# Optimization experiments

Hardware: AMD Instinct MI355X
Metric: run time of the kernel (lower is better)

## Reference

```python
import jax, jax.numpy as jnp
import numpy as np

NUM_HEADS = 16
DEPTH = 0


def rotate_half(x):
    x1, x2 = jnp.split(x, 2, axis=-1)
    return jnp.concatenate((-x2, x1), axis=-1)


def rotary_tables(seq_len, rot_dim, dtype):
    # RotaryEmbedding(dim=rot_dim): inv_freq over even indices of rot_dim
    inv_freq = 1.0 / (10000.0 ** (jnp.arange(0, rot_dim, 2, dtype=jnp.float32) / rot_dim))
    freqs = jnp.arange(seq_len, dtype=jnp.float32)[:, None] * inv_freq[None, :]  # [N, rot_dim/2]
    emb = jnp.concatenate((freqs, freqs), axis=-1)  # [N, rot_dim]
    return emb.astype(dtype), jnp.cos(emb).astype(dtype), jnp.sin(emb).astype(dtype)


def setup_inputs() -> dict:
    key = jax.random.key(0)
    ks = jax.random.split(key, 7)
    B, N, C = 1, 2048, 1024
    hd = C // NUM_HEADS
    std_qkv = (1.0 / C) ** 0.5
    std_proj = (1.0 / (2 * C)) ** 0.5
    return {
        "x": jax.random.normal(ks[0], (B, N, C), dtype=jnp.float32),
        "W_qkv": jax.random.normal(ks[1], (6 * C, C), dtype=jnp.float32) * std_qkv,
        "W_proj": jax.random.normal(ks[2], (C, 2 * C), dtype=jnp.float32) * std_proj,
        "lambda_q1": jax.random.normal(ks[3], (hd,), dtype=jnp.float32) * 0.1,
        "lambda_q2": jax.random.normal(ks[4], (hd,), dtype=jnp.float32) * 0.1,
        "lambda_k1": jax.random.normal(ks[5], (hd,), dtype=jnp.float32) * 0.1,
        "lambda_k2": jax.random.normal(ks[6], (hd,), dtype=jnp.float32) * 0.1,
    }


def reference(x, W_qkv, W_proj, lambda_q1, lambda_q2, lambda_k1, lambda_k2):
    B, N, C = x.shape
    H = NUM_HEADS
    hd = C // H
    scale = hd ** -0.5
    lambda_init = 0.8 - 0.6 * np.exp(-0.3 * DEPTH)

    qkv = jnp.einsum('bnc,dc->bnd', x, W_qkv)               # [B,N,6C]
    qkv = qkv.reshape(B, N, 6, H, hd).transpose(2, 0, 3, 1, 4)  # [6,B,H,N,hd]
    q = jnp.concatenate((qkv[0], qkv[1]), axis=-1)          # [B,H,N,2hd]
    k = jnp.concatenate((qkv[2], qkv[3]), axis=-1)
    v = jnp.concatenate((qkv[4], qkv[5]), axis=-1)

    _, cos, sin = rotary_tables(N, 2 * hd, x.dtype)          # [N,2hd]
    q = q * cos + rotate_half(q) * sin
    k = k * cos + rotate_half(k) * sin

    q1, q2 = jnp.split(q, 2, axis=-1)                        # [B,H,N,hd] each
    k1, k2 = jnp.split(k, 2, axis=-1)

    attn1 = jnp.einsum('bhid,bhjd->bhij', q1, k1) * scale
    attn2 = jnp.einsum('bhid,bhjd->bhij', q2, k2) * scale

    lam1 = jnp.exp(jnp.sum(lambda_q1 * lambda_k1))
    lam2 = jnp.exp(jnp.sum(lambda_q2 * lambda_k2))
    lam = (lam1 - lam2 + lambda_init).astype(x.dtype)

    probs = jax.nn.softmax(attn1, axis=-1) - lam * jax.nn.softmax(attn2, axis=-1)
    out = jnp.einsum('bhij,bhjd->bhid', probs, v)            # [B,H,N,2hd]
    out = out.transpose(0, 2, 1, 3).reshape(B, N, 2 * C)
    out = jnp.einsum('bnd,cd->bnc', out, W_proj)             # [B,N,C]
    return out
```

## Files before the change

kernel.cpp:

```cpp
#include <hip/hip_runtime.h>

using bf16_t = __bf16;
typedef __bf16 bf16x4 __attribute__((ext_vector_type(4)));
typedef __bf16 bf16x8 __attribute__((ext_vector_type(8)));
typedef float floatx4 __attribute__((ext_vector_type(4)));

#define MFMA_BF16(a, b, c) __builtin_amdgcn_mfma_f32_16x16x32_bf16((a), (b), (c), 0, 0, 0)

__device__ __forceinline__ void async_ld16(bf16_t* lds_dst, const bf16_t* g_src) {
    __builtin_amdgcn_global_load_lds(
        (const __attribute__((address_space(1))) void*)g_src,
        (__attribute__((address_space(3))) void*)lds_dst, 16, 0, 0);
}

__global__ __launch_bounds__(256) void cast_all(const float* __restrict__ x,
                                                const float* __restrict__ Wqkv,
                                                const float* __restrict__ Wproj,
                                                const float* __restrict__ lq1,
                                                const float* __restrict__ lq2,
                                                const float* __restrict__ lk1,
                                                const float* __restrict__ lk2,
                                                bf16_t* __restrict__ xb,
                                                bf16_t* __restrict__ Wqkvb,
                                                bf16_t* __restrict__ Wprojb,
                                                float* __restrict__ lamp) {
    const int b = blockIdx.x;
    if (b == 5120) {
        int l = threadIdx.x;
        if (l < 64) {
            float p1 = lq1[l] * lk1[l];
            float p2 = lq2[l] * lk2[l];
            #pragma unroll
            for (int d = 1; d < 64; d <<= 1) {
                p1 += __shfl_xor(p1, d);
                p2 += __shfl_xor(p2, d);
            }
            if (l == 0) *lamp = expf(p1) - expf(p2) + 0.2f;
        }
        return;
    }
    const float* src;
    bf16_t* dst;
    size_t i;
    if (b < 1024)      { src = x;     dst = xb;     i = (size_t)b * 256 + threadIdx.x; }
    else if (b < 4096) { src = Wqkv;  dst = Wqkvb;  i = (size_t)(b - 1024) * 256 + threadIdx.x; }
    else               { src = Wproj; dst = Wprojb; i = (size_t)(b - 4096) * 256 + threadIdx.x; }
    const floatx4 a = *(const floatx4*)(src + i * 8);
    const floatx4 c = *(const floatx4*)(src + i * 8 + 4);
    bf16x8 r;
    r[0] = (bf16_t)a[0]; r[1] = (bf16_t)a[1]; r[2] = (bf16_t)a[2]; r[3] = (bf16_t)a[3];
    r[4] = (bf16_t)c[0]; r[5] = (bf16_t)c[1]; r[6] = (bf16_t)c[2]; r[7] = (bf16_t)c[3];
    *(bf16x8*)(dst + i * 8) = r;
}

__global__ __launch_bounds__(256) void gemm_qkv_rot(const bf16_t* __restrict__ A,
                                                    const bf16_t* __restrict__ B,
                                                    bf16_t* __restrict__ Qb,
                                                    bf16_t* __restrict__ Kb,
                                                    bf16_t* __restrict__ Vt) {
    constexpr int K = 1024, BM = 128, BK = 32;
    __shared__ __align__(16) bf16_t As[2][BM * BK];
    __shared__ __align__(16) bf16_t Bs[2][BM * BK];
    const int t = threadIdx.x;
    const int lane = t & 63, wave = t >> 6;
    const int q4 = lane >> 4, m16 = lane & 15;
    const int mblk = blockIdx.y * BM;
    const int p = blockIdx.x >> 4, hh = blockIdx.x & 15;
    const int pbase = p * 2048 + hh * 64;
    const int wr = wave >> 1, wc = wave & 1;

    auto stage = [&](int buf, int k0) {
        #pragma unroll
        for (int rr = 0; rr < 2; ++rr) {
            int f = rr * 256 + t;
            async_ld16(&As[buf][f * 8], &A[(size_t)(mblk + (f >> 2)) * K + k0 + (f & 3) * 8]);
        }
        #pragma unroll
        for (int rr = 0; rr < 2; ++rr) {
            int f = rr * 256 + t;
            int rp = f >> 2, jt = rp >> 4;
            int Brow = pbase + (jt & 1) * 1024 + ((jt >> 1) * 16) + (rp & 15);
            async_ld16(&Bs[buf][f * 8], &B[(size_t)Brow * K + k0 + (f & 3) * 8]);
        }
    };

    floatx4 acc[4][4] = {};
    stage(0, 0);

    for (int it = 0; it < 32; ++it) {
        const int cur = it & 1;
        __syncthreads();
        if (it + 1 < 32) stage(cur ^ 1, (it + 1) * 32);

        bf16x8 a[4], b[4];
        #pragma unroll
        for (int i = 0; i < 4; ++i)
            a[i] = *(const bf16x8*)&As[cur][(wr * 64 + i * 16 + m16) * 32 + q4 * 8];
        #pragma unroll
        for (int j = 0; j < 4; ++j)
            b[j] = *(const bf16x8*)&Bs[cur][(wc * 64 + j * 16 + m16) * 32 + q4 * 8];
        __builtin_amdgcn_s_setprio(1);
        #pragma unroll
        for (int i = 0; i < 4; ++i)
            #pragma unroll
            for (int j = 0; j < 4; ++j)
                acc[i][j] = MFMA_BF16(a[i], b[j], acc[i][j]);
        __builtin_amdgcn_s_setprio(0);
    }

    if (p < 2) {
        bf16_t* dst = (p == 0) ? Qb : Kb;
        #pragma unroll
        for (int i = 0; i < 4; ++i) {
            int mbase = mblk + wr * 64 + i * 16 + q4 * 4;
            #pragma unroll
            for (int jp = 0; jp < 2; ++jp) {
                int e = (wc * 2 + jp) * 16 + m16;
                float invf = exp2f(-(float)e * (13.287712379549449f / 64.0f));
                #pragma unroll
                for (int r = 0; r < 4; ++r) {
                    int m = mbase + r;
                    float sn, cs;
                    sincosf((float)m * invf, &sn, &cs);
                    float v1 = acc[i][2 * jp][r], v2 = acc[i][2 * jp + 1][r];
                    dst[(size_t)(hh * 2048 + m) * 64 + e]        = (bf16_t)(v1 * cs - v2 * sn);
                    dst[(size_t)((16 + hh) * 2048 + m) * 64 + e] = (bf16_t)(v2 * cs + v1 * sn);
                }
            }
        }
    } else {
        #pragma unroll
        for (int i = 0; i < 4; ++i) {
            int mbase = mblk + wr * 64 + i * 16 + q4 * 4;
            #pragma unroll
            for (int j = 0; j < 4; ++j) {
                int inst = j & 1, e = (wc * 2 + (j >> 1)) * 16 + m16;
                bf16x4 pv;
                #pragma unroll
                for (int r = 0; r < 4; ++r) pv[r] = (bf16_t)acc[i][j][r];
                *(bf16x4*)&Vt[(size_t)(hh * 128 + inst * 64 + e) * 2048 + mbase] = pv;
            }
        }
    }
}

template <int BM, int BN, int BK>
__global__ __launch_bounds__(256) void gemm_bt(const bf16_t* __restrict__ A,
                                               const bf16_t* __restrict__ B,
                                               float* __restrict__ C,
                                               int M, int N, int K) {
    constexpr int KC = BK / 32;
    constexpr int CH = BK / 8;
    constexpr int AR = BM * BK / 2048;
    constexpr int BR = BN * BK / 2048;
    __shared__ __align__(16) bf16_t As[2][BM * BK];
    __shared__ __align__(16) bf16_t Bs[2][BN * BK];
    const int t = threadIdx.x;
    const int lane = t & 63, wave = t >> 6;
    const int q4 = lane >> 4, m16 = lane & 15;
    const int mblk = blockIdx.y * BM, nblk = blockIdx.x * BN;
    const int wr = wave >> 1, wc = wave & 1;
    constexpr int WM = BM / 2, WN = BN / 2;
    constexpr int NI = WM / 16, NJ = WN / 16;

    auto stage = [&](int buf, int k0) {
        #pragma unroll
        for (int rr = 0; rr < AR; ++rr) {
            int f = rr * 256 + t;
            async_ld16(&As[buf][f * 8], &A[(size_t)(mblk + f / CH) * K + k0 + (f % CH) * 8]);
        }
        #pragma unroll
        for (int rr = 0; rr < BR; ++rr) {
            int f = rr * 256 + t;
            async_ld16(&Bs[buf][f * 8], &B[(size_t)(nblk + f / CH) * K + k0 + (f % CH) * 8]);
        }
    };

    floatx4 acc[NI][NJ] = {};
    stage(0, 0);

    const int NTK = K / BK;
    for (int it = 0; it < NTK; ++it) {
        const int cur = it & 1;
        __syncthreads();
        if (it + 1 < NTK) stage(cur ^ 1, (it + 1) * BK);

        bf16x8 a[NI][KC], b[NJ][KC];
        #pragma unroll
        for (int i = 0; i < NI; ++i)
            #pragma unroll
            for (int kk = 0; kk < KC; ++kk)
                a[i][kk] = *(const bf16x8*)&As[cur][(wr * WM + i * 16 + m16) * BK + kk * 32 + q4 * 8];
        #pragma unroll
        for (int j = 0; j < NJ; ++j)
            #pragma unroll
            for (int kk = 0; kk < KC; ++kk)
                b[j][kk] = *(const bf16x8*)&Bs[cur][(wc * WN + j * 16 + m16) * BK + kk * 32 + q4 * 8];
        __builtin_amdgcn_s_setprio(1);
        #pragma unroll
        for (int i = 0; i < NI; ++i)
            #pragma unroll
            for (int j = 0; j < NJ; ++j)
                #pragma unroll
                for (int kk = 0; kk < KC; ++kk)
                    acc[i][j] = MFMA_BF16(a[i][kk], b[j][kk], acc[i][j]);
        __builtin_amdgcn_s_setprio(0);
    }

    #pragma unroll
    for (int i = 0; i < NI; ++i)
        #pragma unroll
        for (int j = 0; j < NJ; ++j) {
            int n = nblk + wc * WN + j * 16 + m16;
            int mbase = mblk + wr * WM + i * 16 + q4 * 4;
            #pragma unroll
            for (int r = 0; r < 4; ++r)
                C[(size_t)(mbase + r) * N + n] = acc[i][j][r];
        }
}

__global__ __launch_bounds__(512, 4) void flash_diff(const bf16_t* __restrict__ Qb,
                                                     const bf16_t* __restrict__ Kb,
                                                     const bf16_t* __restrict__ Vt,
                                                     const float* __restrict__ lamp,
                                                     bf16_t* __restrict__ Ao) {
    constexpr int N = 2048, BN = 64, NT = N / BN;
    __shared__ __align__(16) bf16_t smem[40960];
    bf16_t* Pf = smem + 32768;
    const int t = threadIdx.x, lane = t & 63, w = t >> 6;
    const int comp = w >> 2, w4 = w & 3;
    const int q4 = lane >> 4, m16 = lane & 15;
    const int Lb = blockIdx.x;
    const int virt = (Lb & 7) * 64 + (Lb >> 3);
    const int h = virt >> 5, qt = virt & 31;
    const float lam = *lamp;
    const float cexp = 0.125f * 1.4426950408889634f;

    bf16x8 qf[2];
    const int qrow = qt * 64 + w4 * 16 + m16;
    #pragma unroll
    for (int kc = 0; kc < 2; ++kc)
        qf[kc] = *(const bf16x8*)&Qb[(size_t)((comp * 16 + h) * 2048 + qrow) * 64 + kc * 32 + q4 * 8];

    bf16x8 ones;
    #pragma unroll
    for (int j = 0; j < 8; ++j) ones[j] = (bf16_t)1.0f;

    floatx4 O[8] = {};
    floatx4 sm = {};

    auto stage = [&](bf16_t* Kd, bf16_t* Vd, int k0) {
        #pragma unroll
        for (int rr = 0; rr < 4; ++rr) {
            int idx = w * 4 + rr;
            if (idx < 16) {
                int i = idx >> 3, s = (idx >> 1) & 3, half = idx & 1;
                async_ld16(&Kd[idx * 512],
                           &Kb[(size_t)((i * 16 + h) * 2048 + k0 + 16 * s + m16) * 64 + half * 32 + q4 * 8]);
            } else {
                int v = idx - 16, tt = v >> 1, half = v & 1;
                async_ld16(&Vd[v * 512],
                           &Vt[(size_t)(h * 128 + tt * 16 + m16) * 2048 + k0 + half * 32 + q4 * 8]);
            }
        }
    };

    stage(smem, smem + 8192, 0);

    for (int it = 0; it < NT; ++it) {
        const int cur = it & 1;
        bf16_t* Kf = smem + cur * 16384;
        bf16_t* Vf = Kf + 8192;
        __syncthreads();
        if (it + 1 < NT) {
            bf16_t* Kn = smem + (cur ^ 1) * 16384;
            stage(Kn, Kn + 8192, (it + 1) * BN);
        }

        bf16_t* pw = &Pf[w * 1024];
        __builtin_amdgcn_s_setprio(1);
        #pragma unroll
        for (int s = 0; s < 4; ++s) {
            floatx4 sacc = {};
            const bf16x8 kf0 = *(const bf16x8*)&Kf[((comp * 4 + s) * 2 + 0) * 512 + lane * 8];
            const bf16x8 kf1 = *(const bf16x8*)&Kf[((comp * 4 + s) * 2 + 1) * 512 + lane * 8];
            sacc = MFMA_BF16(qf[0], kf0, sacc);
            sacc = MFMA_BF16(qf[1], kf1, sacc);
            __builtin_amdgcn_s_setprio(0);
            const int half = s >> 1, quad = (2 * s + (m16 >> 3)) & 3, jj = m16 & 7;
            #pragma unroll
            for (int r = 0; r < 4; ++r) {
                int u = quad * 16 + q4 * 4 + r;
                pw[half * 512 + (u ^ quad) * 8 + jj] = (bf16_t)exp2f(sacc[r] * cexp);
            }
            __builtin_amdgcn_s_setprio(1);
        }
        __builtin_amdgcn_s_setprio(0);

        bf16x8 pf[2];
        const int ur = lane ^ q4;
        pf[0] = *(const bf16x8*)&pw[0 * 512 + ur * 8];
        pf[1] = *(const bf16x8*)&pw[1 * 512 + ur * 8];
        sm = MFMA_BF16(pf[0], ones, sm);
        sm = MFMA_BF16(pf[1], ones, sm);
        __builtin_amdgcn_s_setprio(1);
        #pragma unroll
        for (int tt = 0; tt < 8; ++tt) {
            const bf16x8 vf0 = *(const bf16x8*)&Vf[(tt * 2 + 0) * 512 + lane * 8];
            const bf16x8 vf1 = *(const bf16x8*)&Vf[(tt * 2 + 1) * 512 + lane * 8];
            O[tt] = MFMA_BF16(pf[0], vf0, O[tt]);
            O[tt] = MFMA_BF16(pf[1], vf1, O[tt]);
        }
        __builtin_amdgcn_s_setprio(0);
    }

    float inv[4];
    #pragma unroll
    for (int r = 0; r < 4; ++r) inv[r] = 1.0f / sm[r];

    float* Ff = (float*)smem;
    __syncthreads();
    if (comp == 1) {
        #pragma unroll
        for (int tt = 0; tt < 8; ++tt) {
            floatx4 val;
            #pragma unroll
            for (int r = 0; r < 4; ++r) val[r] = lam * O[tt][r] * inv[r];
            *(floatx4*)&Ff[((w4 * 128 + tt * 16 + m16) << 4) + q4 * 4] = val;
        }
    }
    __syncthreads();
    if (comp == 0) {
        const int orow = qt * 64 + w4 * 16 + q4 * 4;
        #pragma unroll
        for (int tt = 0; tt < 8; ++tt) {
            const floatx4 v1 = *(const floatx4*)&Ff[((w4 * 128 + tt * 16 + m16) << 4) + q4 * 4];
            #pragma unroll
            for (int r = 0; r < 4; ++r) {
                float val = O[tt][r] * inv[r] - v1[r];
                Ao[(size_t)(orow + r) * 2048 + h * 128 + tt * 16 + m16] = (bf16_t)val;
            }
        }
    }
}

extern "C" void kernel_launch(void* const* d_in, const int* in_sizes, int n_in,
                              void* d_out, int out_size, void* d_ws, size_t ws_size,
                              hipStream_t stream) {
    const float* x     = (const float*)d_in[0];
    const float* Wqkv  = (const float*)d_in[1];
    const float* Wproj = (const float*)d_in[2];
    const float* lq1   = (const float*)d_in[3];
    const float* lq2   = (const float*)d_in[4];
    const float* lk1   = (const float*)d_in[5];
    const float* lk2   = (const float*)d_in[6];
    float* out = (float*)d_out;

    char* ws = (char*)d_ws;
    bf16_t* xb     = (bf16_t*)(ws);
    bf16_t* Ao     = (bf16_t*)(ws);
    bf16_t* Wqkvb  = (bf16_t*)(ws + 4194304);
    bf16_t* Wprojb = (bf16_t*)(ws + 16777216);
    bf16_t* Qb     = (bf16_t*)(ws + 20971520);
    bf16_t* Kb     = (bf16_t*)(ws + 29360128);
    bf16_t* Vt     = (bf16_t*)(ws + 37748736);
    float*  lamp   = (float*)(ws + 46137344);

    cast_all<<<5121, 256, 0, stream>>>(x, Wqkv, Wproj, lq1, lq2, lk1, lk2,
                                       xb, Wqkvb, Wprojb, lamp);
    gemm_qkv_rot<<<dim3(48, 16), 256, 0, stream>>>(xb, Wqkvb, Qb, Kb, Vt);
    flash_diff<<<512, 512, 0, stream>>>(Qb, Kb, Vt, lamp, Ao);
    gemm_bt<64, 32, 64><<<dim3(32, 32), 256, 0, stream>>>(
        Ao, Wprojb, out, 2048, 1024, 2048);
}
```

Measured before the change: 230.8 us.

## Double query rows per wave in flash_diff, halve KV tile to 32

Each wave now handles two 16-row query groups (128 query rows per block) and reuses every K and V fragment loaded from LDS across both groups. The KV tile shrinks from 64 to 32 keys to keep LDS small, and the grid halves to 256 blocks. This cuts K/V global and LDS traffic per query but doubles the register accumulators and gives fewer blocks to fill the CUs, with more loop iterations and barriers.

```diff
diff --git a/kernel.cpp b/kernel.cpp
--- a/kernel.cpp
+++ b/kernel.cpp
@@ -224,76 +224,77 @@
                                                      const bf16_t* __restrict__ Vt,
                                                      const float* __restrict__ lamp,
                                                      bf16_t* __restrict__ Ao) {
-    constexpr int N = 2048, BN = 64, NT = N / BN;
-    __shared__ __align__(16) bf16_t smem[40960];
-    bf16_t* Pf = smem + 32768;
+    constexpr int N = 2048, BN = 32, NT = N / BN;
+    __shared__ __align__(16) bf16_t smem[24576];
+    bf16_t* Pf = smem + 16384;
     const int t = threadIdx.x, lane = t & 63, w = t >> 6;
     const int comp = w >> 2, w4 = w & 3;
     const int q4 = lane >> 4, m16 = lane & 15;
     const int Lb = blockIdx.x;
-    const int virt = (Lb & 7) * 64 + (Lb >> 3);
-    const int h = virt >> 5, qt = virt & 31;
+    const int virt = (Lb & 7) * 32 + (Lb >> 3);
+    const int h = virt >> 4, qt = virt & 15;
     const float lam = *lamp;
     const float cexp = 0.125f * 1.4426950408889634f;
 
-    bf16x8 qf[2];
-    const int qrow = qt * 64 + w4 * 16 + m16;
-    #pragma unroll
-    for (int kc = 0; kc < 2; ++kc)
-        qf[kc] = *(const bf16x8*)&Qb[(size_t)((comp * 16 + h) * 2048 + qrow) * 64 + kc * 32 + q4 * 8];
+    bf16x8 qf[2][2];
+    #pragma unroll
+    for (int g = 0; g < 2; ++g)
+        #pragma unroll
+        for (int kc = 0; kc < 2; ++kc)
+            qf[g][kc] = *(const bf16x8*)&Qb[(size_t)((comp * 16 + h) * 2048 +
+                             qt * 128 + w4 * 32 + g * 16 + m16) * 64 + kc * 32 + q4 * 8];
 
     bf16x8 ones;
     #pragma unroll
     for (int j = 0; j < 8; ++j) ones[j] = (bf16_t)1.0f;
 
-    floatx4 O[8] = {};
-    floatx4 sm = {};
-
-    auto stage = [&](bf16_t* Kd, bf16_t* Vd, int k0) {
-        #pragma unroll
-        for (int rr = 0; rr < 4; ++rr) {
-            int idx = w * 4 + rr;
-            if (idx < 16) {
-                int i = idx >> 3, s = (idx >> 1) & 3, half = idx & 1;
-                async_ld16(&Kd[idx * 512],
+    floatx4 O[2][8] = {};
+    floatx4 sm[2] = {};
+
+    auto stage = [&](bf16_t* buf, int k0) {
+        #pragma unroll
+        for (int rr = 0; rr < 2; ++rr) {
+            int idx = w * 2 + rr;
+            if (idx < 8) {
+                int i = idx >> 2, s = (idx >> 1) & 1, half = idx & 1;
+                async_ld16(&buf[idx * 512],
                            &Kb[(size_t)((i * 16 + h) * 2048 + k0 + 16 * s + m16) * 64 + half * 32 + q4 * 8]);
             } else {
-                int v = idx - 16, tt = v >> 1, half = v & 1;
-                async_ld16(&Vd[v * 512],
-                           &Vt[(size_t)(h * 128 + tt * 16 + m16) * 2048 + k0 + half * 32 + q4 * 8]);
+                int tt = idx - 8;
+                async_ld16(&buf[idx * 512],
+                           &Vt[(size_t)(h * 128 + tt * 16 + m16) * 2048 + k0 + q4 * 8]);
             }
         }
     };
 
-    stage(smem, smem + 8192, 0);
+    stage(smem, 0);
 
     for (int it = 0; it < NT; ++it) {
-        const int cur = it & 1;
-        bf16_t* Kf = smem + cur * 16384;
-        bf16_t* Vf = Kf + 8192;
-        __syncthreads();
-        if (it + 1 < NT) {
-            bf16_t* Kn = smem + (cur ^ 1) * 16384;
-            stage(Kn, Kn + 8192, (it + 1) * BN);
-        }
+        bf16_t* buf = smem + (it & 1) * 8192;
+        bf16_t* Vf = buf + 4096;
+        __syncthreads();
+        if (it + 1 < NT) stage(smem + (((it & 1) ^ 1) * 8192), (it + 1) * BN);
 
         bf16_t* pw = &Pf[w * 1024];
         __builtin_amdgcn_s_setprio(1);
         #pragma unroll
-        for (int s = 0; s < 4; ++s) {
-            floatx4 sacc = {};
-            const bf16x8 kf0 = *(const bf16x8*)&Kf[((comp * 4 + s) * 2 + 0) * 512 + lane * 8];
-            const bf16x8 kf1 = *(const bf16x8*)&Kf[((comp * 4 + s) * 2 + 1) * 512 + lane * 8];
-            sacc = MFMA_BF16(qf[0], kf0, sacc);
-            sacc = MFMA_BF16(qf[1], kf1, sacc);
-            __builtin_amdgcn_s_setprio(0);
-            const int half = s >> 1, quad = (2 * s + (m16 >> 3)) & 3, jj = m16 & 7;
-            #pragma unroll
-            for (int r = 0; r < 4; ++r) {
-                int u = quad * 16 + q4 * 4 + r;
-                pw[half * 512 + (u ^ quad) * 8 + jj] = (bf16_t)exp2f(sacc[r] * cexp);
-            }
-            __builtin_amdgcn_s_setprio(1);
+        for (int g = 0; g < 2; ++g) {
+            #pragma unroll
+            for (int s = 0; s < 2; ++s) {
+                floatx4 sacc = {};
+                const bf16x8 kf0 = *(const bf16x8*)&buf[((comp * 2 + s) * 2 + 0) * 512 + lane * 8];
+                const bf16x8 kf1 = *(const bf16x8*)&buf[((comp * 2 + s) * 2 + 1) * 512 + lane * 8];
+                sacc = MFMA_BF16(qf[g][0], kf0, sacc);
+                sacc = MFMA_BF16(qf[g][1], kf1, sacc);
+                __builtin_amdgcn_s_setprio(0);
+                const int quad = (2 * s + (m16 >> 3)) & 3, jj = m16 & 7;
+                #pragma unroll
+                for (int r = 0; r < 4; ++r) {
+                    int u = quad * 16 + q4 * 4 + r;
+                    pw[g * 512 + (u ^ quad) * 8 + jj] = (bf16_t)exp2f(sacc[r] * cexp);
+                }
+                __builtin_amdgcn_s_setprio(1);
+            }
         }
         __builtin_amdgcn_s_setprio(0);
 
@@ -301,44 +302,48 @@
         const int ur = lane ^ q4;
         pf[0] = *(const bf16x8*)&pw[0 * 512 + ur * 8];
         pf[1] = *(const bf16x8*)&pw[1 * 512 + ur * 8];
-        sm = MFMA_BF16(pf[0], ones, sm);
-        sm = MFMA_BF16(pf[1], ones, sm);
+        sm[0] = MFMA_BF16(pf[0], ones, sm[0]);
+        sm[1] = MFMA_BF16(pf[1], ones, sm[1]);
         __builtin_amdgcn_s_setprio(1);
         #pragma unroll
         for (int tt = 0; tt < 8; ++tt) {
-            const bf16x8 vf0 = *(const bf16x8*)&Vf[(tt * 2 + 0) * 512 + lane * 8];
-            const bf16x8 vf1 = *(const bf16x8*)&Vf[(tt * 2 + 1) * 512 + lane * 8];
-            O[tt] = MFMA_BF16(pf[0], vf0, O[tt]);
-            O[tt] = MFMA_BF16(pf[1], vf1, O[tt]);
+            const bf16x8 vf = *(const bf16x8*)&Vf[tt * 512 + lane * 8];
+            O[0][tt] = MFMA_BF16(pf[0], vf, O[0][tt]);
+            O[1][tt] = MFMA_BF16(pf[1], vf, O[1][tt]);
         }
         __builtin_amdgcn_s_setprio(0);
     }
 
-    float inv[4];
-    #pragma unroll
-    for (int r = 0; r < 4; ++r) inv[r] = 1.0f / sm[r];
+    float inv[2][4];
+    #pragma unroll
+    for (int g = 0; g < 2; ++g)
+        #pragma unroll
+        for (int r = 0; r < 4; ++r) inv[g][r] = 1.0f / sm[g][r];
 
     float* Ff = (float*)smem;
-    __syncthreads();
-    if (comp == 1) {
-        #pragma unroll
-        for (int tt = 0; tt < 8; ++tt) {
-            floatx4 val;
-            #pragma unroll
-            for (int r = 0; r < 4; ++r) val[r] = lam * O[tt][r] * inv[r];
-            *(floatx4*)&Ff[((w4 * 128 + tt * 16 + m16) << 4) + q4 * 4] = val;
-        }
-    }
-    __syncthreads();
-    if (comp == 0) {
-        const int orow = qt * 64 + w4 * 16 + q4 * 4;
-        #pragma unroll
-        for (int tt = 0; tt < 8; ++tt) {
-            const floatx4 v1 = *(const floatx4*)&Ff[((w4 * 128 + tt * 16 + m16) << 4) + q4 * 4];
-            #pragma unroll
-            for (int r = 0; r < 4; ++r) {
-                float val = O[tt][r] * inv[r] - v1[r];
-                Ao[(size_t)(orow + r) * 2048 + h * 128 + tt * 16 + m16] = (bf16_t)val;
+    #pragma unroll
+    for (int g = 0; g < 2; ++g) {
+        __syncthreads();
+        if (comp == 1) {
+            #pragma unroll
+            for (int tt = 0; tt < 8; ++tt) {
+                floatx4 val;
+                #pragma unroll
+                for (int r = 0; r < 4; ++r) val[r] = lam * O[g][tt][r] * inv[g][r];
+                *(floatx4*)&Ff[((w4 * 128 + tt * 16 + m16) << 4) + q4 * 4] = val;
+            }
+        }
+        __syncthreads();
+        if (comp == 0) {
+            const int orow = qt * 128 + w4 * 32 + g * 16 + q4 * 4;
+            #pragma unroll
+            for (int tt = 0; tt < 8; ++tt) {
+                const floatx4 v1 = *(const floatx4*)&Ff[((w4 * 128 + tt * 16 + m16) << 4) + q4 * 4];
+                #pragma unroll
+                for (int r = 0; r < 4; ++r) {
+                    float val = O[g][tt][r] * inv[g][r] - v1[r];
+                    Ao[(size_t)(orow + r) * 2048 + h * 128 + tt * 16 + m16] = (bf16_t)val;
+                }
             }
         }
     }
@@ -369,7 +374,7 @@
     cast_all<<<5121, 256, 0, stream>>>(x, Wqkv, Wproj, lq1, lq2, lk1, lk2,
                                        xb, Wqkvb, Wprojb, lamp);
     gemm_qkv_rot<<<dim3(48, 16), 256, 0, stream>>>(xb, Wqkvb, Qb, Kb, Vt);
-    flash_diff<<<512, 512, 0, stream>>>(Qb, Kb, Vt, lamp, Ao);
+    flash_diff<<<256, 512, 0, stream>>>(Qb, Kb, Vt, lamp, Ao);
     gemm_bt<64, 32, 64><<<dim3(32, 32), 256, 0, stream>>>(
         Ao, Wprojb, out, 2048, 1024, 2048);
 }
```

New measurement: 237.1 us. +2.7%, slower.
